# Kernel optimization log

Measured on AMD Instinct MI355X. Metric: run time of the kernel, lower is better.

The kernel has to match this reference:

```python
import jax, jax.numpy as jnp
import numpy as np

EPS = 1e-9
N_HEAD = 16


def clamp_c(c):
    return jnp.clip(c, 1e-4, 1.0)


def _heads(x, H):
    B, T, C = x.shape
    return x.reshape(B, T, H, C // H)


def mobius_add(x, y, c_clamped, H):
    # per-head Mobius addition; c_clamped: (H,)
    B, T, C = x.shape
    cr = c_clamped.reshape(1, 1, H, 1)
    xr, yr = _heads(x, H), _heads(y, H)
    xn = jnp.sum(xr * xr, axis=-1, keepdims=True)
    yn = jnp.sum(yr * yr, axis=-1, keepdims=True)
    ip = jnp.sum(xr * yr, axis=-1, keepdims=True)
    num = (1 + 2 * cr * ip + cr * yn) * xr + (1 - cr * xn) * yr
    den = 1 + 2 * cr * ip + cr ** 2 * xn * yn
    return (num / (den + EPS)).reshape(B, T, C)


def expmap(x, v, c, H):
    # exponential map of tangent vector v at point x (per-head curvature)
    B, T, C = x.shape
    cc = clamp_c(c)
    cr = cc.reshape(1, 1, H, 1)
    xr, vr = _heads(x, H), _heads(v, H)
    sf = 2.0 / (1 + cr * jnp.sum(xr * xr, axis=-1, keepdims=True) + EPS)  # scaling factor
    vns = jnp.sum(vr * vr, axis=-1, keepdims=True)
    vn = jnp.sqrt(vns + EPS)
    tanh_arg = jnp.abs(cr * sf * vns / 2)
    coeff = (1.0 / (jnp.sqrt(jnp.abs(cr) + EPS) + EPS)) * jnp.tanh(jnp.sqrt(tanh_arg + EPS))
    second = (coeff * vr / (vn + EPS)).reshape(B, T, C)
    return mobius_add(x, second, cc, H)


def layernorm(x, g):
    m = jnp.mean(x, axis=-1, keepdims=True)
    v = jnp.mean((x - m) ** 2, axis=-1, keepdims=True)
    return (x - m) * jax.lax.rsqrt(v + 1e-5) * g


def attention(x, w_qkv, w_proj, H):
    B, T, C = x.shape
    hs = C // H
    q, k, v = jnp.split(x @ w_qkv.T, 3, axis=-1)
    q = q.reshape(B, T, H, hs).transpose(0, 2, 1, 3)
    k = k.reshape(B, T, H, hs).transpose(0, 2, 1, 3)
    v = v.reshape(B, T, H, hs).transpose(0, 2, 1, 3)
    att = jnp.einsum('bhqd,bhkd->bhqk', q, k) * (float(hs) ** -0.5)
    mask = jnp.tril(jnp.ones((T, T), dtype=bool))
    att = jnp.where(mask, att, -jnp.inf)
    att = jax.nn.softmax(att, axis=-1)
    y = jnp.einsum('bhqk,bhkd->bhqd', att, v)
    y = y.transpose(0, 2, 1, 3).reshape(B, T, C)
    return y @ w_proj.T


def setup_inputs() -> dict:
    key = jax.random.key(0)
    ks = jax.random.split(key, 9)
    B, T, C = 2, 2048, 1024
    s = 0.02
    return {
        'x': jax.random.normal(ks[0], (B, T, C), jnp.float32) * s,
        'ln1_g': jnp.ones((C,), jnp.float32),
        'w_qkv': jax.random.normal(ks[1], (3 * C, C), jnp.float32) * s,
        'w_attn_proj': jax.random.normal(ks[2], (C, C), jnp.float32) * s,
        'c_attn': jax.random.uniform(ks[3], (N_HEAD,), jnp.float32, 0.1, 0.9),
        'ln2_g': jnp.ones((C,), jnp.float32),
        'w_fc': jax.random.normal(ks[4], (4 * C, C), jnp.float32) * s,
        'w_mlp_proj': jax.random.normal(ks[5], (C, 4 * C), jnp.float32) * s,
        'c_mlp': jax.random.uniform(ks[6], (N_HEAD,), jnp.float32, 0.1, 0.9),
    }


def reference(x, ln1_g, w_qkv, w_attn_proj, c_attn, ln2_g, w_fc, w_mlp_proj, c_mlp):
    H = N_HEAD
    a = attention(layernorm(x, ln1_g), w_qkv, w_attn_proj, H)
    x = expmap(x, a, c_attn, H)  # hyperbolic residual (attn)
    h = jax.nn.gelu(layernorm(x, ln2_g) @ w_fc.T, approximate=False) @ w_mlp_proj.T
    x = expmap(x, h, c_mlp, H)   # hyperbolic residual (mlp)
    return x
```

## Files before the change

kernel.cpp:

```cpp
#include <hip/hip_runtime.h>
#include <hip/hip_bf16.h>

typedef __attribute__((ext_vector_type(8))) short bf16x8;
typedef __attribute__((ext_vector_type(4))) float f32x4;

typedef const __attribute__((address_space(1))) void gv_t;
typedef __attribute__((address_space(3))) void lv_t;
#define GLL16(g, l) __builtin_amdgcn_global_load_lds((gv_t*)(g), (lv_t*)(l), 16, 0, 0)

#define WAITV8() asm volatile("s_waitcnt vmcnt(8)" ::: "memory")
#define WAITV0() asm volatile("s_waitcnt vmcnt(0)" ::: "memory")
#define WAITL0() asm volatile("s_waitcnt lgkmcnt(0)" ::: "memory")
#define SCHEDB() __builtin_amdgcn_sched_barrier(0)
#define BARRAW() __builtin_amdgcn_s_barrier()

__device__ __forceinline__ short f2bf(float f) {
    __hip_bfloat16 h = __float2bfloat16(f);
    return *reinterpret_cast<short*>(&h);
}

__device__ __forceinline__ float wred(float v) {
    #pragma unroll
    for (int m = 1; m < 64; m <<= 1) v += __shfl_xor(v, m);
    return v;
}

__global__ __launch_bounds__(256) void cvt_kernel(const float* __restrict__ in,
                                                  short* __restrict__ out, int n4) {
    int i = blockIdx.x * 256 + threadIdx.x;
    if (i < n4) {
        float4 v = ((const float4*)in)[i];
        short4 o;
        o.x = f2bf(v.x); o.y = f2bf(v.y); o.z = f2bf(v.z); o.w = f2bf(v.w);
        ((short4*)out)[i] = o;
    }
}

__global__ __launch_bounds__(256) void ln_kernel(const float* __restrict__ x,
                                                 const float* __restrict__ g,
                                                 short* __restrict__ y) {
    const int row = blockIdx.x, tid = threadIdx.x;
    const float4 v = ((const float4*)(x + (size_t)row * 1024))[tid];
    float s = v.x + v.y + v.z + v.w;
    float s2 = v.x * v.x + v.y * v.y + v.z * v.z + v.w * v.w;
    #pragma unroll
    for (int m = 1; m < 64; m <<= 1) { s += __shfl_xor(s, m); s2 += __shfl_xor(s2, m); }
    __shared__ float rs[4], rs2[4];
    if ((tid & 63) == 0) { rs[tid >> 6] = s; rs2[tid >> 6] = s2; }
    __syncthreads();
    s = rs[0] + rs[1] + rs[2] + rs[3];
    s2 = rs2[0] + rs2[1] + rs2[2] + rs2[3];
    const float mean = s * (1.0f / 1024.0f);
    const float var = s2 * (1.0f / 1024.0f) - mean * mean;
    const float r = rsqrtf(var + 1e-5f);
    const float4 gg = ((const float4*)g)[tid];
    short4 o;
    o.x = f2bf((v.x - mean) * r * gg.x);
    o.y = f2bf((v.y - mean) * r * gg.y);
    o.z = f2bf((v.z - mean) * r * gg.z);
    o.w = f2bf((v.w - mean) * r * gg.w);
    ((short4*)y)[(size_t)row * 256 + tid] = o;
}

template <int EPI>
__global__ __launch_bounds__(256, 2) void gemm_bt(const short* __restrict__ A,
                                                  const short* __restrict__ Bw,
                                                  int M, int N, int K,
                                                  void* __restrict__ o0,
                                                  void* __restrict__ o1,
                                                  void* __restrict__ o2) {
    __shared__ __align__(16) short As[2][128 * 64];
    __shared__ __align__(16) short Bs[2][128 * 64];
    const int tid = threadIdx.x;
    const int wid = tid >> 6, lane = tid & 63;
    const int wm = wid >> 1, wn = wid & 1;
    const int col = lane & 15, grp = lane >> 4;
    const int r8 = lane >> 3, s8 = lane & 7;
    const int m0 = blockIdx.x * 128, n0 = blockIdx.y * 128;
    f32x4 acc[4][4] = {};
    const short* ga = A + (size_t)m0 * K;
    const short* gb = Bw + (size_t)n0 * K;

#define GSTAGE(b_, t_) do {                                                     \
        const int k0_ = (t_) * 64;                                              \
        _Pragma("unroll")                                                       \
        for (int c = 0; c < 4; ++c) {                                           \
            const int row = c * 32 + wid * 8 + r8;                              \
            const int slot = s8 ^ (row & 7);                                    \
            GLL16(ga + (size_t)row * K + k0_ + slot * 8,                        \
                  (char*)&As[b_][0] + c * 4096 + wid * 1024);                   \
            GLL16(gb + (size_t)row * K + k0_ + slot * 8,                        \
                  (char*)&Bs[b_][0] + c * 4096 + wid * 1024);                   \
        }                                                                       \
    } while (0)

    const int NT = K >> 6;
    GSTAGE(0, 0);
    if (NT > 1) { GSTAGE(1, 1); WAITV8(); } else { WAITV0(); }
    SCHEDB();
    BARRAW();
    int cur = 0;
    for (int t = 0; t < NT; ++t) {
        const char* At = (const char*)&As[cur][0];
        const char* Bt = (const char*)&Bs[cur][0];
        bf16x8 af[2][4], bfr[2][4];
        #pragma unroll
        for (int s = 0; s < 2; ++s)
            #pragma unroll
            for (int i = 0; i < 4; ++i) {
                const int rowA = wm * 64 + i * 16 + col;
                const int rowB = wn * 64 + i * 16 + col;
                af[s][i]  = *(const bf16x8*)(At + rowA * 128 + (((s * 4 + grp) ^ (rowA & 7)) << 4));
                bfr[s][i] = *(const bf16x8*)(Bt + rowB * 128 + (((s * 4 + grp) ^ (rowB & 7)) << 4));
            }
        WAITL0(); SCHEDB();
        BARRAW();
        if (t + 2 < NT) GSTAGE(cur, t + 2);
        #pragma unroll
        for (int s = 0; s < 2; ++s)
            #pragma unroll
            for (int mi = 0; mi < 4; ++mi)
                #pragma unroll
                for (int ni = 0; ni < 4; ++ni)
                    acc[mi][ni] = __builtin_amdgcn_mfma_f32_16x16x32_bf16(af[s][mi], bfr[s][ni], acc[mi][ni], 0, 0, 0);
        if (t + 1 < NT) {
            if (t + 2 < NT) { WAITV8(); } else { WAITV0(); }
            SCHEDB();
            BARRAW();
        }
        cur ^= 1;
    }
#undef GSTAGE
    #pragma unroll
    for (int mi = 0; mi < 4; ++mi) {
        #pragma unroll
        for (int ni = 0; ni < 4; ++ni) {
            #pragma unroll
            for (int i = 0; i < 4; ++i) {
                const int m = m0 + wm * 64 + mi * 16 + grp * 4 + i;
                const int n = n0 + wn * 64 + ni * 16 + col;
                const float v = acc[mi][ni][i];
                if (EPI == 0) {
                    const int b = m >> 11, t = m & 2047;
                    const int which = n >> 10, nn = n & 1023;
                    const int h = nn >> 6, d = nn & 63;
                    const size_t bh = (size_t)(b * 16 + h);
                    if (which == 0)
                        ((short*)o0)[(bh * 2048 + t) * 64 + d] = f2bf(v * 0.125f);
                    else if (which == 1)
                        ((short*)o1)[(bh * 2048 + t) * 64 + d] = f2bf(v);
                    else
                        ((short*)o2)[(bh * 64 + d) * 2048 + t] = f2bf(v);
                } else if (EPI == 1) {
                    ((float*)o0)[(size_t)m * N + n] = v;
                } else {
                    const float gl = 0.5f * v * (1.0f + erff(v * 0.70710678118654752f));
                    ((short*)o0)[(size_t)m * N + n] = f2bf(gl);
                }
            }
        }
    }
}

__global__ __launch_bounds__(256, 3) void attn_kernel(const short* __restrict__ Q,
                                                      const short* __restrict__ Kg,
                                                      const short* __restrict__ VT,
                                                      short* __restrict__ Y) {
    __shared__ __align__(16) short Ks[2][4096];
    __shared__ __align__(16) short Vs[2][4096];
    __shared__ __align__(16) short Plds[4][16 * 72];
    const int j = 15 - blockIdx.x;
    const int bh = blockIdx.y;
    const int tid = threadIdx.x, wid = tid >> 6, lane = tid & 63;
    const int ql = lane & 15, g = lane >> 4;
    const int r8 = lane >> 3, s8 = lane & 7;
    const int q0w = j * 128 + wid * 32;
    const int lt = 2 * j + 1;
    const short* Qb = Q + (size_t)bh * 2048 * 64;
    const short* Kb = Kg + (size_t)bh * 2048 * 64;
    const short* Vb = VT + (size_t)bh * 64 * 2048;
    short* Pw = &Plds[wid][0];

    bf16x8 qf[2][2];
    #pragma unroll
    for (int qs = 0; qs < 2; ++qs) {
        qf[qs][0] = *(const bf16x8*)&Qb[(size_t)(q0w + 16 * qs + ql) * 64 + 8 * g];
        qf[qs][1] = *(const bf16x8*)&Qb[(size_t)(q0w + 16 * qs + ql) * 64 + 32 + 8 * g];
    }
    f32x4 o[2][4] = {};
    float m[2] = {-1e30f, -1e30f}, lsum[2] = {0.f, 0.f};

#define STAGE(b_, kt_) do {                                                      \
        const int kbase_ = (kt_) * 64;                                           \
        _Pragma("unroll")                                                        \
        for (int c = 0; c < 2; ++c) {                                            \
            const int row = c * 32 + wid * 8 + r8;                               \
            const int slot = s8 ^ (row & 7);                                     \
            GLL16(Kb + (size_t)(kbase_ + row) * 64 + slot * 8,                   \
                  (char*)&Ks[b_][0] + c * 4096 + wid * 1024);                    \
            GLL16(Vb + (size_t)row * 2048 + kbase_ + slot * 8,                   \
                  (char*)&Vs[b_][0] + c * 4096 + wid * 1024);                    \
        }                                                                        \
    } while (0)

    STAGE(0, 0);
    __syncthreads();
    int buf = 0;
    for (int kt = 0; kt <= lt; ++kt) {
        if (kt < lt) STAGE(buf ^ 1, kt + 1);
        const int kbase = kt * 64;
        const short* Kt = &Ks[buf][0];
        const short* Vt = &Vs[buf][0];
        bf16x8 kf[4][2];
        #pragma unroll
        for (int kb = 0; kb < 4; ++kb) {
            const int row = 16 * kb + ql;
            const int x = row & 7;
            kf[kb][0] = *(const bf16x8*)((const char*)Kt + row * 128 + ((g ^ x) << 4));
            kf[kb][1] = *(const bf16x8*)((const char*)Kt + row * 128 + (((4 + g) ^ x) << 4));
        }
        #pragma unroll
        for (int qs = 0; qs < 2; ++qs) {
            const int q0s = q0w + 16 * qs;
            if (kbase > q0s + 15) continue;
            f32x4 s[4];
            #pragma unroll
            for (int kb = 0; kb < 4; ++kb) {
                f32x4 z = {0.f, 0.f, 0.f, 0.f};
                z = __builtin_amdgcn_mfma_f32_16x16x32_bf16(kf[kb][0], qf[qs][0], z, 0, 0, 0);
                z = __builtin_amdgcn_mfma_f32_16x16x32_bf16(kf[kb][1], qf[qs][1], z, 0, 0, 0);
                s[kb] = z;
            }
            if (kbase + 63 > q0s) {
                #pragma unroll
                for (int kb = 0; kb < 4; ++kb)
                    #pragma unroll
                    for (int r = 0; r < 4; ++r)
                        if (kbase + 16 * kb + 4 * g + r > q0s + ql) s[kb][r] = -1e30f;
            }
            float t0 = fmaxf(fmaxf(s[0][0], s[0][1]), fmaxf(s[0][2], s[0][3]));
            float t1 = fmaxf(fmaxf(s[1][0], s[1][1]), fmaxf(s[1][2], s[1][3]));
            float t2 = fmaxf(fmaxf(s[2][0], s[2][1]), fmaxf(s[2][2], s[2][3]));
            float t3 = fmaxf(fmaxf(s[3][0], s[3][1]), fmaxf(s[3][2], s[3][3]));
            float tmax = fmaxf(fmaxf(t0, t1), fmaxf(t2, t3));
            tmax = fmaxf(tmax, __shfl_xor(tmax, 16));
            tmax = fmaxf(tmax, __shfl_xor(tmax, 32));
            const float mnew = fmaxf(m[qs], tmax);
            const float sc = __expf(m[qs] - mnew);
            m[qs] = mnew;
            float rsum = 0.0f;
            #pragma unroll
            for (int kb = 0; kb < 4; ++kb) {
                const float e0 = __expf(s[kb][0] - mnew);
                const float e1 = __expf(s[kb][1] - mnew);
                const float e2 = __expf(s[kb][2] - mnew);
                const float e3 = __expf(s[kb][3] - mnew);
                rsum += (e0 + e1) + (e2 + e3);
                short4 pk;
                pk.x = f2bf(e0); pk.y = f2bf(e1); pk.z = f2bf(e2); pk.w = f2bf(e3);
                *(short4*)&Pw[ql * 72 + 16 * kb + 4 * g] = pk;
            }
            rsum += __shfl_xor(rsum, 16);
            rsum += __shfl_xor(rsum, 32);
            lsum[qs] = lsum[qs] * sc + rsum;
            #pragma unroll
            for (int nf = 0; nf < 4; ++nf)
                #pragma unroll
                for (int r = 0; r < 4; ++r) o[qs][nf][r] *= sc;
            const bf16x8 pb0 = *(const bf16x8*)&Pw[ql * 72 + 8 * g];
            const bf16x8 pb1 = *(const bf16x8*)&Pw[ql * 72 + 32 + 8 * g];
            #pragma unroll
            for (int nf = 0; nf < 4; ++nf) {
                const int row = 16 * nf + ql;
                const int x = row & 7;
                bf16x8 v0 = *(const bf16x8*)((const char*)Vt + row * 128 + ((g ^ x) << 4));
                bf16x8 v1 = *(const bf16x8*)((const char*)Vt + row * 128 + (((4 + g) ^ x) << 4));
                o[qs][nf] = __builtin_amdgcn_mfma_f32_16x16x32_bf16(v0, pb0, o[qs][nf], 0, 0, 0);
                o[qs][nf] = __builtin_amdgcn_mfma_f32_16x16x32_bf16(v1, pb1, o[qs][nf], 0, 0, 0);
            }
        }
        __syncthreads();
        buf ^= 1;
    }
#undef STAGE
    const int b = bh >> 4, h = bh & 15;
    #pragma unroll
    for (int qs = 0; qs < 2; ++qs) {
        const float inv = 1.0f / lsum[qs];
        const size_t rowoff = ((size_t)b * 2048 + q0w + 16 * qs + ql) * 1024 + h * 64;
        #pragma unroll
        for (int nf = 0; nf < 4; ++nf) {
            short4 w;
            w.x = f2bf(o[qs][nf][0] * inv);
            w.y = f2bf(o[qs][nf][1] * inv);
            w.z = f2bf(o[qs][nf][2] * inv);
            w.w = f2bf(o[qs][nf][3] * inv);
            *(short4*)&Y[rowoff + 16 * nf + 4 * g] = w;
        }
    }
}

__global__ __launch_bounds__(256) void expmap_kernel(const float* __restrict__ x,
                                                     const float* __restrict__ v,
                                                     const float* __restrict__ carr,
                                                     float* __restrict__ out) {
    const int blk = blockIdx.x;
    const int row = blk >> 2;
    const int head = (blk & 3) * 4 + (threadIdx.x >> 6);
    const int lane = threadIdx.x & 63;
    const size_t idx = (size_t)row * 1024 + head * 64 + lane;
    float c = carr[head];
    c = fminf(fmaxf(c, 1e-4f), 1.0f);
    const float xe = x[idx], ve = v[idx];
    const float xn = wred(xe * xe);
    const float vns = wred(ve * ve);
    const float vn = sqrtf(vns + 1e-9f);
    const float sf = 2.0f / (1.0f + c * xn + 1e-9f);
    const float targ = fabsf(0.5f * c * sf * vns);
    const float coeff = (1.0f / (sqrtf(c + 1e-9f) + 1e-9f)) * tanhf(sqrtf(targ + 1e-9f));
    const float ye = coeff * ve / (vn + 1e-9f);
    const float yn = wred(ye * ye);
    const float ip = wred(xe * ye);
    const float num = (1.0f + 2.0f * c * ip + c * yn) * xe + (1.0f - c * xn) * ye;
    const float den = 1.0f + 2.0f * c * ip + c * c * xn * yn;
    out[idx] = num / (den + 1e-9f);
}

extern "C" void kernel_launch(void* const* d_in, const int* in_sizes, int n_in,
                              void* d_out, int out_size, void* d_ws, size_t ws_size,
                              hipStream_t stream) {
    (void)in_sizes; (void)n_in; (void)out_size; (void)ws_size;
    const float* x      = (const float*)d_in[0];
    const float* ln1_g  = (const float*)d_in[1];
    const float* w_qkv  = (const float*)d_in[2];
    const float* w_proj = (const float*)d_in[3];
    const float* c_attn = (const float*)d_in[4];
    const float* ln2_g  = (const float*)d_in[5];
    const float* w_fc   = (const float*)d_in[6];
    const float* w_mlp  = (const float*)d_in[7];
    const float* c_mlp  = (const float*)d_in[8];
    float* out = (float*)d_out;
    char* ws = (char*)d_ws;
    const size_t MB = 1024 * 1024;

    short* wqkv_bf  = (short*)(ws + 0 * MB);
    short* wproj_bf = (short*)(ws + 6 * MB);
    short* wfc_bf   = (short*)(ws + 8 * MB);
    short* wmlp_bf  = (short*)(ws + 16 * MB);
    short* y_bf     = (short*)(ws + 24 * MB);
    short* q_bf     = (short*)(ws + 32 * MB);
    short* k_bf     = (short*)(ws + 40 * MB);
    short* vT_bf    = (short*)(ws + 48 * MB);
    short* att_bf   = (short*)(ws + 56 * MB);
    float* a_f32    = (float*)(ws + 64 * MB);
    float* x1       = (float*)(ws + 80 * MB);
    short* g_bf     = (short*)(ws + 32 * MB);
    float* h_f32    = (float*)(ws + 64 * MB);

    cvt_kernel<<<3072, 256, 0, stream>>>(w_qkv, wqkv_bf, 3072 * 1024 / 4);
    cvt_kernel<<<1024, 256, 0, stream>>>(w_proj, wproj_bf, 1024 * 1024 / 4);
    cvt_kernel<<<4096, 256, 0, stream>>>(w_fc, wfc_bf, 4096 * 1024 / 4);
    cvt_kernel<<<4096, 256, 0, stream>>>(w_mlp, wmlp_bf, 1024 * 4096 / 4);

    ln_kernel<<<4096, 256, 0, stream>>>(x, ln1_g, y_bf);
    gemm_bt<0><<<dim3(32, 24), 256, 0, stream>>>(y_bf, wqkv_bf, 4096, 3072, 1024,
                                                 q_bf, k_bf, vT_bf);
    attn_kernel<<<dim3(16, 32), 256, 0, stream>>>(q_bf, k_bf, vT_bf, att_bf);
    gemm_bt<1><<<dim3(32, 8), 256, 0, stream>>>(att_bf, wproj_bf, 4096, 1024, 1024,
                                                a_f32, nullptr, nullptr);
    expmap_kernel<<<16384, 256, 0, stream>>>(x, a_f32, c_attn, x1);
    ln_kernel<<<4096, 256, 0, stream>>>(x1, ln2_g, y_bf);
    gemm_bt<2><<<dim3(32, 32), 256, 0, stream>>>(y_bf, wfc_bf, 4096, 4096, 1024,
                                                 g_bf, nullptr, nullptr);
    gemm_bt<1><<<dim3(32, 8), 256, 0, stream>>>(g_bf, wmlp_bf, 4096, 1024, 4096,
                                                h_f32, nullptr, nullptr);
    expmap_kernel<<<16384, 256, 0, stream>>>(x1, h_f32, c_mlp, out);
}
```

Before: 303.1 us.

## Widen GEMM tiles to 128x256, split-K projections, and shrink attention query blocks

The GEMM now uses 128x256 output tiles with 4x8 MFMA accumulators per wave. It splits its first half-K MFMAs ahead of the barrier so LDS reads overlap compute. The two N=1024 projection GEMMs use split-K over two z slices writing separate fp32 partials, which the expmap kernel sums on load. The attention kernel now uses 64-query blocks (16 queries per wave) with twice as many blocks, aiming for better load balance and occupancy. The trade-offs are higher register pressure with launch_bounds min-blocks removed, extra partial-sum traffic, and reshuffled workspace aliasing.

```diff
diff --git a/kernel.cpp b/kernel.cpp
--- a/kernel.cpp
+++ b/kernel.cpp
@@ -8,11 +8,11 @@
 typedef __attribute__((address_space(3))) void lv_t;
 #define GLL16(g, l) __builtin_amdgcn_global_load_lds((gv_t*)(g), (lv_t*)(l), 16, 0, 0)
 
-#define WAITV8() asm volatile("s_waitcnt vmcnt(8)" ::: "memory")
-#define WAITV0() asm volatile("s_waitcnt vmcnt(0)" ::: "memory")
-#define WAITL0() asm volatile("s_waitcnt lgkmcnt(0)" ::: "memory")
-#define SCHEDB() __builtin_amdgcn_sched_barrier(0)
-#define BARRAW() __builtin_amdgcn_s_barrier()
+#define WAITV12() asm volatile("s_waitcnt vmcnt(12)" ::: "memory")
+#define WAITV0()  asm volatile("s_waitcnt vmcnt(0)" ::: "memory")
+#define WAITL0()  asm volatile("s_waitcnt lgkmcnt(0)" ::: "memory")
+#define SCHEDB()  __builtin_amdgcn_sched_barrier(0)
+#define BARRAW()  __builtin_amdgcn_s_barrier()
 
 __device__ __forceinline__ short f2bf(float f) {
     __hip_bfloat16 h = __float2bfloat16(f);
@@ -63,23 +63,24 @@
 }
 
 template <int EPI>
-__global__ __launch_bounds__(256, 2) void gemm_bt(const short* __restrict__ A,
-                                                  const short* __restrict__ Bw,
-                                                  int M, int N, int K,
-                                                  void* __restrict__ o0,
-                                                  void* __restrict__ o1,
-                                                  void* __restrict__ o2) {
+__global__ __launch_bounds__(256) void gemm_bt(const short* __restrict__ A,
+                                               const short* __restrict__ Bw,
+                                               int M, int N, int LDK, int KL,
+                                               void* __restrict__ o0,
+                                               void* __restrict__ o1,
+                                               void* __restrict__ o2) {
     __shared__ __align__(16) short As[2][128 * 64];
-    __shared__ __align__(16) short Bs[2][128 * 64];
+    __shared__ __align__(16) short Bs[2][256 * 64];
     const int tid = threadIdx.x;
     const int wid = tid >> 6, lane = tid & 63;
     const int wm = wid >> 1, wn = wid & 1;
     const int col = lane & 15, grp = lane >> 4;
     const int r8 = lane >> 3, s8 = lane & 7;
-    const int m0 = blockIdx.x * 128, n0 = blockIdx.y * 128;
-    f32x4 acc[4][4] = {};
-    const short* ga = A + (size_t)m0 * K;
-    const short* gb = Bw + (size_t)n0 * K;
+    const int m0 = blockIdx.x * 128, n0 = blockIdx.y * 256;
+    const int z = blockIdx.z;
+    f32x4 acc[4][8] = {};
+    const short* ga = A + (size_t)m0 * LDK + (size_t)z * KL;
+    const short* gb = Bw + (size_t)n0 * LDK + (size_t)z * KL;
 
 #define GSTAGE(b_, t_) do {                                                     \
         const int k0_ = (t_) * 64;                                              \
@@ -87,44 +88,64 @@
         for (int c = 0; c < 4; ++c) {                                           \
             const int row = c * 32 + wid * 8 + r8;                              \
             const int slot = s8 ^ (row & 7);                                    \
-            GLL16(ga + (size_t)row * K + k0_ + slot * 8,                        \
+            GLL16(ga + (size_t)row * LDK + k0_ + slot * 8,                      \
                   (char*)&As[b_][0] + c * 4096 + wid * 1024);                   \
-            GLL16(gb + (size_t)row * K + k0_ + slot * 8,                        \
+        }                                                                       \
+        _Pragma("unroll")                                                       \
+        for (int c = 0; c < 8; ++c) {                                           \
+            const int row = c * 32 + wid * 8 + r8;                              \
+            const int slot = s8 ^ (row & 7);                                    \
+            GLL16(gb + (size_t)row * LDK + k0_ + slot * 8,                      \
                   (char*)&Bs[b_][0] + c * 4096 + wid * 1024);                   \
         }                                                                       \
     } while (0)
 
-    const int NT = K >> 6;
+    const int NT = KL >> 6;
     GSTAGE(0, 0);
-    if (NT > 1) { GSTAGE(1, 1); WAITV8(); } else { WAITV0(); }
-    SCHEDB();
+    GSTAGE(1, 1);
+    WAITV12(); SCHEDB();
     BARRAW();
     int cur = 0;
     for (int t = 0; t < NT; ++t) {
         const char* At = (const char*)&As[cur][0];
         const char* Bt = (const char*)&Bs[cur][0];
-        bf16x8 af[2][4], bfr[2][4];
-        #pragma unroll
-        for (int s = 0; s < 2; ++s)
-            #pragma unroll
-            for (int i = 0; i < 4; ++i) {
-                const int rowA = wm * 64 + i * 16 + col;
-                const int rowB = wn * 64 + i * 16 + col;
-                af[s][i]  = *(const bf16x8*)(At + rowA * 128 + (((s * 4 + grp) ^ (rowA & 7)) << 4));
-                bfr[s][i] = *(const bf16x8*)(Bt + rowB * 128 + (((s * 4 + grp) ^ (rowB & 7)) << 4));
-            }
+        bf16x8 af0[4], bf0[8];
+        #pragma unroll
+        for (int i = 0; i < 4; ++i) {
+            const int rowA = wm * 64 + i * 16 + col;
+            af0[i] = *(const bf16x8*)(At + rowA * 128 + ((grp ^ (rowA & 7)) << 4));
+        }
+        #pragma unroll
+        for (int jn = 0; jn < 8; ++jn) {
+            const int rowB = wn * 128 + jn * 16 + col;
+            bf0[jn] = *(const bf16x8*)(Bt + rowB * 128 + ((grp ^ (rowB & 7)) << 4));
+        }
+        #pragma unroll
+        for (int mi = 0; mi < 4; ++mi)
+            #pragma unroll
+            for (int nj = 0; nj < 8; ++nj)
+                acc[mi][nj] = __builtin_amdgcn_mfma_f32_16x16x32_bf16(af0[mi], bf0[nj], acc[mi][nj], 0, 0, 0);
+        bf16x8 af1[4], bf1[8];
+        #pragma unroll
+        for (int i = 0; i < 4; ++i) {
+            const int rowA = wm * 64 + i * 16 + col;
+            af1[i] = *(const bf16x8*)(At + rowA * 128 + (((4 + grp) ^ (rowA & 7)) << 4));
+        }
+        #pragma unroll
+        for (int jn = 0; jn < 8; ++jn) {
+            const int rowB = wn * 128 + jn * 16 + col;
+            bf1[jn] = *(const bf16x8*)(Bt + rowB * 128 + (((4 + grp) ^ (rowB & 7)) << 4));
+        }
         WAITL0(); SCHEDB();
         BARRAW();
         if (t + 2 < NT) GSTAGE(cur, t + 2);
         #pragma unroll
-        for (int s = 0; s < 2; ++s)
-            #pragma unroll
-            for (int mi = 0; mi < 4; ++mi)
-                #pragma unroll
-                for (int ni = 0; ni < 4; ++ni)
-                    acc[mi][ni] = __builtin_amdgcn_mfma_f32_16x16x32_bf16(af[s][mi], bfr[s][ni], acc[mi][ni], 0, 0, 0);
+        for (int mi = 0; mi < 4; ++mi)
+            #pragma unroll
+            for (int nj = 0; nj < 8; ++nj)
+                acc[mi][nj] = __builtin_amdgcn_mfma_f32_16x16x32_bf16(af1[mi], bf1[nj], acc[mi][nj], 0, 0, 0);
         if (t + 1 < NT) {
-            if (t + 2 < NT) { WAITV8(); } else { WAITV0(); }
+            if (t + 2 < NT) { WAITV12(); } else { WAITV0(); }
             SCHEDB();
             BARRAW();
         }
@@ -134,12 +155,12 @@
     #pragma unroll
     for (int mi = 0; mi < 4; ++mi) {
         #pragma unroll
-        for (int ni = 0; ni < 4; ++ni) {
+        for (int nj = 0; nj < 8; ++nj) {
             #pragma unroll
             for (int i = 0; i < 4; ++i) {
                 const int m = m0 + wm * 64 + mi * 16 + grp * 4 + i;
-                const int n = n0 + wn * 64 + ni * 16 + col;
-                const float v = acc[mi][ni][i];
+                const int n = n0 + wn * 128 + nj * 16 + col;
+                const float v = acc[mi][nj][i];
                 if (EPI == 0) {
                     const int b = m >> 11, t = m & 2047;
                     const int which = n >> 10, nn = n & 1023;
@@ -152,7 +173,8 @@
                     else
                         ((short*)o2)[(bh * 64 + d) * 2048 + t] = f2bf(v);
                 } else if (EPI == 1) {
-                    ((float*)o0)[(size_t)m * N + n] = v;
+                    float* dst = (z == 0) ? (float*)o0 : (float*)o1;
+                    dst[(size_t)m * N + n] = v;
                 } else {
                     const float gl = 0.5f * v * (1.0f + erff(v * 0.70710678118654752f));
                     ((short*)o0)[(size_t)m * N + n] = f2bf(gl);
@@ -169,26 +191,22 @@
     __shared__ __align__(16) short Ks[2][4096];
     __shared__ __align__(16) short Vs[2][4096];
     __shared__ __align__(16) short Plds[4][16 * 72];
-    const int j = 15 - blockIdx.x;
+    const int j = 31 - blockIdx.x;
     const int bh = blockIdx.y;
     const int tid = threadIdx.x, wid = tid >> 6, lane = tid & 63;
     const int ql = lane & 15, g = lane >> 4;
     const int r8 = lane >> 3, s8 = lane & 7;
-    const int q0w = j * 128 + wid * 32;
-    const int lt = 2 * j + 1;
+    const int q0s = j * 64 + wid * 16;
+    const int lt = j;
     const short* Qb = Q + (size_t)bh * 2048 * 64;
     const short* Kb = Kg + (size_t)bh * 2048 * 64;
     const short* Vb = VT + (size_t)bh * 64 * 2048;
     short* Pw = &Plds[wid][0];
 
-    bf16x8 qf[2][2];
-    #pragma unroll
-    for (int qs = 0; qs < 2; ++qs) {
-        qf[qs][0] = *(const bf16x8*)&Qb[(size_t)(q0w + 16 * qs + ql) * 64 + 8 * g];
-        qf[qs][1] = *(const bf16x8*)&Qb[(size_t)(q0w + 16 * qs + ql) * 64 + 32 + 8 * g];
-    }
-    f32x4 o[2][4] = {};
-    float m[2] = {-1e30f, -1e30f}, lsum[2] = {0.f, 0.f};
+    bf16x8 qf0 = *(const bf16x8*)&Qb[(size_t)(q0s + ql) * 64 + 8 * g];
+    bf16x8 qf1 = *(const bf16x8*)&Qb[(size_t)(q0s + ql) * 64 + 32 + 8 * g];
+    f32x4 o[4] = {};
+    float m = -1e30f, lsum = 0.0f;
 
 #define STAGE(b_, kt_) do {                                                      \
         const int kbase_ = (kt_) * 64;                                           \
@@ -219,89 +237,82 @@
             kf[kb][0] = *(const bf16x8*)((const char*)Kt + row * 128 + ((g ^ x) << 4));
             kf[kb][1] = *(const bf16x8*)((const char*)Kt + row * 128 + (((4 + g) ^ x) << 4));
         }
-        #pragma unroll
-        for (int qs = 0; qs < 2; ++qs) {
-            const int q0s = q0w + 16 * qs;
-            if (kbase > q0s + 15) continue;
-            f32x4 s[4];
-            #pragma unroll
-            for (int kb = 0; kb < 4; ++kb) {
-                f32x4 z = {0.f, 0.f, 0.f, 0.f};
-                z = __builtin_amdgcn_mfma_f32_16x16x32_bf16(kf[kb][0], qf[qs][0], z, 0, 0, 0);
-                z = __builtin_amdgcn_mfma_f32_16x16x32_bf16(kf[kb][1], qf[qs][1], z, 0, 0, 0);
-                s[kb] = z;
-            }
-            if (kbase + 63 > q0s) {
+        f32x4 s[4];
+        #pragma unroll
+        for (int kb = 0; kb < 4; ++kb) {
+            f32x4 z = {0.f, 0.f, 0.f, 0.f};
+            z = __builtin_amdgcn_mfma_f32_16x16x32_bf16(kf[kb][0], qf0, z, 0, 0, 0);
+            z = __builtin_amdgcn_mfma_f32_16x16x32_bf16(kf[kb][1], qf1, z, 0, 0, 0);
+            s[kb] = z;
+        }
+        if (kbase + 63 > q0s) {
+            #pragma unroll
+            for (int kb = 0; kb < 4; ++kb)
                 #pragma unroll
-                for (int kb = 0; kb < 4; ++kb)
-                    #pragma unroll
-                    for (int r = 0; r < 4; ++r)
-                        if (kbase + 16 * kb + 4 * g + r > q0s + ql) s[kb][r] = -1e30f;
-            }
-            float t0 = fmaxf(fmaxf(s[0][0], s[0][1]), fmaxf(s[0][2], s[0][3]));
-            float t1 = fmaxf(fmaxf(s[1][0], s[1][1]), fmaxf(s[1][2], s[1][3]));
-            float t2 = fmaxf(fmaxf(s[2][0], s[2][1]), fmaxf(s[2][2], s[2][3]));
-            float t3 = fmaxf(fmaxf(s[3][0], s[3][1]), fmaxf(s[3][2], s[3][3]));
-            float tmax = fmaxf(fmaxf(t0, t1), fmaxf(t2, t3));
-            tmax = fmaxf(tmax, __shfl_xor(tmax, 16));
-            tmax = fmaxf(tmax, __shfl_xor(tmax, 32));
-            const float mnew = fmaxf(m[qs], tmax);
-            const float sc = __expf(m[qs] - mnew);
-            m[qs] = mnew;
-            float rsum = 0.0f;
-            #pragma unroll
-            for (int kb = 0; kb < 4; ++kb) {
-                const float e0 = __expf(s[kb][0] - mnew);
-                const float e1 = __expf(s[kb][1] - mnew);
-                const float e2 = __expf(s[kb][2] - mnew);
-                const float e3 = __expf(s[kb][3] - mnew);
-                rsum += (e0 + e1) + (e2 + e3);
-                short4 pk;
-                pk.x = f2bf(e0); pk.y = f2bf(e1); pk.z = f2bf(e2); pk.w = f2bf(e3);
-                *(short4*)&Pw[ql * 72 + 16 * kb + 4 * g] = pk;
-            }
-            rsum += __shfl_xor(rsum, 16);
-            rsum += __shfl_xor(rsum, 32);
-            lsum[qs] = lsum[qs] * sc + rsum;
-            #pragma unroll
-            for (int nf = 0; nf < 4; ++nf)
-                #pragma unroll
-                for (int r = 0; r < 4; ++r) o[qs][nf][r] *= sc;
-            const bf16x8 pb0 = *(const bf16x8*)&Pw[ql * 72 + 8 * g];
-            const bf16x8 pb1 = *(const bf16x8*)&Pw[ql * 72 + 32 + 8 * g];
-            #pragma unroll
-            for (int nf = 0; nf < 4; ++nf) {
-                const int row = 16 * nf + ql;
-                const int x = row & 7;
-                bf16x8 v0 = *(const bf16x8*)((const char*)Vt + row * 128 + ((g ^ x) << 4));
-                bf16x8 v1 = *(const bf16x8*)((const char*)Vt + row * 128 + (((4 + g) ^ x) << 4));
-                o[qs][nf] = __builtin_amdgcn_mfma_f32_16x16x32_bf16(v0, pb0, o[qs][nf], 0, 0, 0);
-                o[qs][nf] = __builtin_amdgcn_mfma_f32_16x16x32_bf16(v1, pb1, o[qs][nf], 0, 0, 0);
-            }
+                for (int r = 0; r < 4; ++r)
+                    if (kbase + 16 * kb + 4 * g + r > q0s + ql) s[kb][r] = -1e30f;
+        }
+        float t0 = fmaxf(fmaxf(s[0][0], s[0][1]), fmaxf(s[0][2], s[0][3]));
+        float t1 = fmaxf(fmaxf(s[1][0], s[1][1]), fmaxf(s[1][2], s[1][3]));
+        float t2 = fmaxf(fmaxf(s[2][0], s[2][1]), fmaxf(s[2][2], s[2][3]));
+        float t3 = fmaxf(fmaxf(s[3][0], s[3][1]), fmaxf(s[3][2], s[3][3]));
+        float tmax = fmaxf(fmaxf(t0, t1), fmaxf(t2, t3));
+        tmax = fmaxf(tmax, __shfl_xor(tmax, 16));
+        tmax = fmaxf(tmax, __shfl_xor(tmax, 32));
+        const float mnew = fmaxf(m, tmax);
+        const float sc = __expf(m - mnew);
+        m = mnew;
+        float rsum = 0.0f;
+        #pragma unroll
+        for (int kb = 0; kb < 4; ++kb) {
+            const float e0 = __expf(s[kb][0] - mnew);
+            const float e1 = __expf(s[kb][1] - mnew);
+            const float e2 = __expf(s[kb][2] - mnew);
+            const float e3 = __expf(s[kb][3] - mnew);
+            rsum += (e0 + e1) + (e2 + e3);
+            short4 pk;
+            pk.x = f2bf(e0); pk.y = f2bf(e1); pk.z = f2bf(e2); pk.w = f2bf(e3);
+            *(short4*)&Pw[ql * 72 + 16 * kb + 4 * g] = pk;
+        }
+        rsum += __shfl_xor(rsum, 16);
+        rsum += __shfl_xor(rsum, 32);
+        lsum = lsum * sc + rsum;
+        #pragma unroll
+        for (int nf = 0; nf < 4; ++nf)
+            #pragma unroll
+            for (int r = 0; r < 4; ++r) o[nf][r] *= sc;
+        const bf16x8 pb0 = *(const bf16x8*)&Pw[ql * 72 + 8 * g];
+        const bf16x8 pb1 = *(const bf16x8*)&Pw[ql * 72 + 32 + 8 * g];
+        #pragma unroll
+        for (int nf = 0; nf < 4; ++nf) {
+            const int row = 16 * nf + ql;
+            const int x = row & 7;
+            bf16x8 v0 = *(const bf16x8*)((const char*)Vt + row * 128 + ((g ^ x) << 4));
+            bf16x8 v1 = *(const bf16x8*)((const char*)Vt + row * 128 + (((4 + g) ^ x) << 4));
+            o[nf] = __builtin_amdgcn_mfma_f32_16x16x32_bf16(v0, pb0, o[nf], 0, 0, 0);
+            o[nf] = __builtin_amdgcn_mfma_f32_16x16x32_bf16(v1, pb1, o[nf], 0, 0, 0);
         }
         __syncthreads();
         buf ^= 1;
     }
 #undef STAGE
     const int b = bh >> 4, h = bh & 15;
+    const float inv = 1.0f / lsum;
+    const size_t rowoff = ((size_t)b * 2048 + q0s + ql) * 1024 + h * 64;
     #pragma unroll
-    for (int qs = 0; qs < 2; ++qs) {
-        const float inv = 1.0f / lsum[qs];
-        const size_t rowoff = ((size_t)b * 2048 + q0w + 16 * qs + ql) * 1024 + h * 64;
-        #pragma unroll
-        for (int nf = 0; nf < 4; ++nf) {
-            short4 w;
-            w.x = f2bf(o[qs][nf][0] * inv);
-            w.y = f2bf(o[qs][nf][1] * inv);
-            w.z = f2bf(o[qs][nf][2] * inv);
-            w.w = f2bf(o[qs][nf][3] * inv);
-            *(short4*)&Y[rowoff + 16 * nf + 4 * g] = w;
-        }
+    for (int nf = 0; nf < 4; ++nf) {
+        short4 w;
+        w.x = f2bf(o[nf][0] * inv);
+        w.y = f2bf(o[nf][1] * inv);
+        w.z = f2bf(o[nf][2] * inv);
+        w.w = f2bf(o[nf][3] * inv);
+        *(short4*)&Y[rowoff + 16 * nf + 4 * g] = w;
     }
 }
 
 __global__ __launch_bounds__(256) void expmap_kernel(const float* __restrict__ x,
-                                                     const float* __restrict__ v,
+                                                     const float* __restrict__ va,
+                                                     const float* __restrict__ vb,
                                                      const float* __restrict__ carr,
                                                      float* __restrict__ out) {
     const int blk = blockIdx.x;
@@ -311,7 +322,7 @@
     const size_t idx = (size_t)row * 1024 + head * 64 + lane;
     float c = carr[head];
     c = fminf(fmaxf(c, 1e-4f), 1.0f);
-    const float xe = x[idx], ve = v[idx];
+    const float xe = x[idx], ve = va[idx] + vb[idx];
     const float xn = wred(xe * xe);
     const float vns = wred(ve * ve);
     const float vn = sqrtf(vns + 1e-9f);
@@ -352,10 +363,12 @@
     short* k_bf     = (short*)(ws + 40 * MB);
     short* vT_bf    = (short*)(ws + 48 * MB);
     short* att_bf   = (short*)(ws + 56 * MB);
-    float* a_f32    = (float*)(ws + 64 * MB);
-    float* x1       = (float*)(ws + 80 * MB);
-    short* g_bf     = (short*)(ws + 32 * MB);
-    float* h_f32    = (float*)(ws + 64 * MB);
+    float* a0       = (float*)(ws + 64 * MB);
+    float* a1       = (float*)(ws + 80 * MB);
+    float* x1       = (float*)(ws + 40 * MB);
+    short* g_bf     = (short*)(ws + 56 * MB);
+    float* h0       = (float*)(ws + 0 * MB);
+    float* h1       = (float*)(ws + 24 * MB);
 
     cvt_kernel<<<3072, 256, 0, stream>>>(w_qkv, wqkv_bf, 3072 * 1024 / 4);
     cvt_kernel<<<1024, 256, 0, stream>>>(w_proj, wproj_bf, 1024 * 1024 / 4);
@@ -363,16 +376,16 @@
     cvt_kernel<<<4096, 256, 0, stream>>>(w_mlp, wmlp_bf, 1024 * 4096 / 4);
 
     ln_kernel<<<4096, 256, 0, stream>>>(x, ln1_g, y_bf);
-    gemm_bt<0><<<dim3(32, 24), 256, 0, stream>>>(y_bf, wqkv_bf, 4096, 3072, 1024,
-                                                 q_bf, k_bf, vT_bf);
-    attn_kernel<<<dim3(16, 32), 256, 0, stream>>>(q_bf, k_bf, vT_bf, att_bf);
-    gemm_bt<1><<<dim3(32, 8), 256, 0, stream>>>(att_bf, wproj_bf, 4096, 1024, 1024,
-                                                a_f32, nullptr, nullptr);
-    expmap_kernel<<<16384, 256, 0, stream>>>(x, a_f32, c_attn, x1);
+    gemm_bt<0><<<dim3(32, 12, 1), 256, 0, stream>>>(y_bf, wqkv_bf, 4096, 3072, 1024, 1024,
+                                                    q_bf, k_bf, vT_bf);
+    attn_kernel<<<dim3(32, 32), 256, 0, stream>>>(q_bf, k_bf, vT_bf, att_bf);
+    gemm_bt<1><<<dim3(32, 4, 2), 256, 0, stream>>>(att_bf, wproj_bf, 4096, 1024, 1024, 512,
+                                                   a0, a1, nullptr);
+    expmap_kernel<<<16384, 256, 0, stream>>>(x, a0, a1, c_attn, x1);
     ln_kernel<<<4096, 256, 0, stream>>>(x1, ln2_g, y_bf);
-    gemm_bt<2><<<dim3(32, 32), 256, 0, stream>>>(y_bf, wfc_bf, 4096, 4096, 1024,
-                                                 g_bf, nullptr, nullptr);
-    gemm_bt<1><<<dim3(32, 8), 256, 0, stream>>>(g_bf, wmlp_bf, 4096, 1024, 4096,
-                                                h_f32, nullptr, nullptr);
-    expmap_kernel<<<16384, 256, 0, stream>>>(x1, h_f32, c_mlp, out);
-}
+    gemm_bt<2><<<dim3(32, 16, 1), 256, 0, stream>>>(y_bf, wfc_bf, 4096, 4096, 1024, 1024,
+                                                    g_bf, nullptr, nullptr);
+    gemm_bt<1><<<dim3(32, 4, 2), 256, 0, stream>>>(g_bf, wmlp_bf, 4096, 1024, 4096, 2048,
+                                                   h0, h1, nullptr);
+    expmap_kernel<<<16384, 256, 0, stream>>>(x1, h0, h1, c_mlp, out);
+}
```

Result: slower. 445.1 us (+46.8%).
